# Performance work log

Hardware: AMD Instinct MI355X
Metric: run time of the kernel (lower is better)

## Reference

```python
import jax, jax.numpy as jnp
import numpy as np

V, OOV, E, HE, HD, B, S, T = 50000, 100, 128, 256, 256, 32, 256, 16
NEG = -1e20


def lstm(x, W, U, b, h0, c0):
    # x: [B, L, F]; standard (Keras-style i,f,g,o) LSTM via scan over time
    def step(carry, xt):
        h, c = carry
        z = xt @ W + h @ U + b
        i, f, g, o = jnp.split(z, 4, axis=-1)
        c = jax.nn.sigmoid(f) * c + jax.nn.sigmoid(i) * jnp.tanh(g)
        h = jax.nn.sigmoid(o) * jnp.tanh(c)
        return (h, c), h
    (h, c), hs = jax.lax.scan(step, (h0, c0), jnp.swapaxes(x, 0, 1))
    return jnp.swapaxes(hs, 0, 1), h, c


def setup_inputs() -> dict:
    key = jax.random.key(0)
    ks = jax.random.split(key, 16)
    g = lambda i, shape: jax.random.normal(ks[i], shape, dtype=jnp.float32) * 0.05
    return {
        'x': jax.random.randint(ks[0], (B, S), 0, V),
        'x_with_oov': jax.random.randint(ks[1], (B, S), 0, V + OOV),
        'x_len': jax.random.randint(ks[2], (B,), 1, S + 1),
        'dec_x': jax.random.randint(ks[3], (B, T), 0, V),
        'embedding': g(4, (V, E)),
        'Wenc': g(5, (E, 4 * HE)), 'Uenc': g(6, (HE, 4 * HE)), 'benc': jnp.zeros(4 * HE, jnp.float32),
        'We2d': g(7, (HE, HD)), 'be2d': jnp.zeros(HD, jnp.float32),
        'Wdec': g(8, (E, 4 * HD)), 'Udec': g(9, (HD, 4 * HD)), 'bdec': jnp.zeros(4 * HD, jnp.float32),
        'Wattn': g(10, (HD, HE)),
        'Wout': g(11, (HE + HD, HD)), 'bout': jnp.zeros(HD, jnp.float32),
        'Wgen': g(12, (HD, V)),
        'Wcopy': g(13, (HE, HD)), 'bcopy': jnp.zeros(HD, jnp.float32),
    }


def reference(x, x_with_oov, x_len, dec_x, embedding, Wenc, Uenc, benc,
              We2d, be2d, Wdec, Udec, bdec, Wattn, Wout, bout, Wgen, Wcopy, bcopy):
    # Encoder (unidirectional; Keras encoder ignores mask in this branch)
    enc_out, eh, ec = lstm(embedding[x], Wenc, Uenc, benc,
                           jnp.zeros((B, HE), embedding.dtype), jnp.zeros((B, HE), embedding.dtype))
    # NOTE: source applies encoder2decoder_state to BOTH h and c (faithful)
    h0 = eh @ We2d + be2d
    c0 = ec @ We2d + be2d
    # Decoder LSTM
    dec_out, sh, sc = lstm(embedding[dec_x], Wdec, Udec, bdec, h0, c0)  # [B,T,HD]
    mask = jnp.arange(S)[None, :] < x_len[:, None]                      # [B,S]
    # Attention (score_mode='general')
    scores = jnp.einsum('bth,he,bse->bts', dec_out, Wattn, enc_out)     # [B,T,S]
    scores = jnp.where(mask[:, None, :], scores, NEG)
    aw = jax.nn.softmax(scores, axis=2)
    ctx = jnp.einsum('bts,bse->bte', aw, enc_out)                       # [B,T,HE]
    attn_out = jnp.tanh(jnp.concatenate([ctx, dec_out], axis=-1) @ Wout + bout)  # [B,T,HD]
    # Generation scores, padded with tiny constant over OOV slots
    gen = jnp.exp(attn_out @ Wgen)                                      # [B,T,V]
    gen = jnp.pad(gen, ((0, 0), (0, 0), (0, OOV)), constant_values=1e-10)
    # Copy scores over source positions, scattered into extended vocab
    copy_seq = jnp.einsum('bsh,bth->bts', jnp.tanh(enc_out @ Wcopy + bcopy), attn_out)
    copy_seq = jnp.exp(jnp.where(mask[:, None, :], copy_seq, NEG))      # [B,T,S]
    b_idx = jnp.arange(B)[:, None, None]
    t_idx = jnp.arange(T)[None, :, None]
    v_idx = x_with_oov[:, None, :]                                      # broadcast to [B,T,S]
    copy_vocab = jnp.zeros((B, T, V + OOV), gen.dtype).at[b_idx, t_idx, v_idx].add(copy_seq)
    total = gen + copy_vocab
    log_prob = jnp.log(total / jnp.sum(total, axis=2, keepdims=True))
    return log_prob, sh, sc
```

## Files before the change

kernel.cpp:

```cpp
#include <hip/hip_runtime.h>

#define V_   50000
#define OOV_ 100
#define VO_  50100
#define E_   128
#define HE_  256
#define HD_  256
#define B_   32
#define S_   256
#define T_   16

typedef _Float16 h2_t __attribute__((ext_vector_type(2)));
typedef __attribute__((ext_vector_type(8))) short bfrag_t;
typedef __attribute__((ext_vector_type(4))) float f32x4;
typedef unsigned short ushort_t;

union U32H2 { unsigned u; h2_t h; };
union FRAG  { uint4 u; bfrag_t s; };

static __device__ __forceinline__ float bf2f(unsigned short b) {
  return __uint_as_float(((unsigned)b) << 16);
}
static __device__ __forceinline__ unsigned short f2bf(float f) {
  unsigned u = __float_as_uint(f);
  unsigned r = (u + 0x7fffu + ((u >> 16) & 1u)) >> 16;
  return (unsigned short)r;
}
static __device__ __forceinline__ float sigm(float x) { return 1.f / (1.f + expf(-x)); }

static __device__ __forceinline__ float dot2u(unsigned upair, unsigned hpairv, float acc) {
  U32H2 a; a.u = upair;
  U32H2 b; b.u = hpairv;
#if __has_builtin(__builtin_amdgcn_fdot2)
  return __builtin_amdgcn_fdot2(a.h, b.h, acc, false);
#else
  acc = fmaf((float)a.h.x, (float)b.h.x, acc);
  return fmaf((float)a.h.y, (float)b.h.y, acc);
#endif
}

__global__ __launch_bounds__(256) void mfma_gemm(
    const ushort_t* __restrict__ A, const ushort_t* __restrict__ Bt,
    const float* __restrict__ bias, float* __restrict__ C, ushort_t* __restrict__ Cbf,
    float* __restrict__ rsum, int M, int N, int K, int ldC, int act)
{
  const int w = threadIdx.x >> 6, lane = threadIdx.x & 63;
  const int m0 = blockIdx.y * 64 + w * 16;
  const int n0 = blockIdx.x * 64;
  const int l16 = lane & 15, lq = lane >> 4;
  f32x4 acc[4] = {f32x4{0,0,0,0}, f32x4{0,0,0,0}, f32x4{0,0,0,0}, f32x4{0,0,0,0}};
  for (int k0 = 0; k0 < K; k0 += 32) {
    FRAG a;
    a.u = *(const uint4*)(A + (size_t)(m0 + l16) * K + k0 + lq * 8);
#pragma unroll
    for (int ns = 0; ns < 4; ns++) {
      int n = n0 + ns * 16 + l16;
      int nc = n < N ? n : N - 1;
      FRAG bf;
      bf.u = *(const uint4*)(Bt + (size_t)nc * K + k0 + lq * 8);
      acc[ns] = __builtin_amdgcn_mfma_f32_16x16x32_bf16(a.s, bf.s, acc[ns], 0, 0, 0);
    }
  }
  float bv[4];
#pragma unroll
  for (int ns = 0; ns < 4; ns++) {
    int col = n0 + ns * 16 + l16;
    bv[ns] = (bias && col < N) ? bias[col] : 0.f;
  }
#pragma unroll
  for (int r = 0; r < 4; r++) {
    int row = m0 + lq * 4 + r;
    float part = 0.f;
#pragma unroll
    for (int ns = 0; ns < 4; ns++) {
      int col = n0 + ns * 16 + l16;
      if (col < N) {
        float v = acc[ns][r] + bv[ns];
        if (act == 1) v = tanhf(v);
        else if (act == 2) v = expf(v);
        if (Cbf) Cbf[(size_t)row * ldC + col] = f2bf(v);
        else     C[(size_t)row * ldC + col] = v;
        part += v;
      }
    }
    if (rsum) {
      part += __shfl_xor(part, 1);
      part += __shfl_xor(part, 2);
      part += __shfl_xor(part, 4);
      part += __shfl_xor(part, 8);
      if (l16 == 0) atomicAdd(&rsum[row], part);
    }
  }
}

static __device__ __forceinline__ void tconv_tile(
    const float* __restrict__ W, ushort_t* __restrict__ Wt, int K, int N,
    int kb, int nb, int tid, ushort_t (*tile)[33])
{
  const int tx = tid & 31, ty = tid >> 5;
#pragma unroll
  for (int p = 0; p < 4; p++) {
    int k = kb + ty + p * 8, n = nb + tx;
    if (k < K && n < N) tile[ty + p * 8][tx] = f2bf(W[(size_t)k * N + n]);
  }
  __syncthreads();
#pragma unroll
  for (int p = 0; p < 4; p++) {
    int n = nb + ty + p * 8, k = kb + tx;
    if (k < K && n < N) Wt[(size_t)n * K + k] = tile[tx][ty + p * 8];
  }
}
static __device__ __forceinline__ void packU2_one(
    const float* __restrict__ U, unsigned* __restrict__ out, int i)
{
  int p = i >> 10, col = i & 1023;
  U32H2 cv; cv.h = h2_t{(_Float16)U[(size_t)(2 * p) * 1024 + col],
                        (_Float16)U[(size_t)(2 * p + 1) * 1024 + col]};
  out[i] = cv.u;
}

__global__ __launch_bounds__(256) void prep_kernel(
    const float* __restrict__ Wenc, const float* __restrict__ Wdec,
    const float* __restrict__ We2d, const float* __restrict__ Wattn,
    const float* __restrict__ Wout, const float* __restrict__ Wcopy,
    const float* __restrict__ Uenc, const float* __restrict__ Udec,
    const int* __restrict__ x, const int* __restrict__ decx, const float* __restrict__ emb,
    ushort_t* WencT, ushort_t* WdecT, ushort_t* We2dT, ushort_t* WattnT,
    ushort_t* WoutT, ushort_t* WcopyT, unsigned* Upk2E, unsigned* Upk2D,
    ushort_t* xembbf, ushort_t* dembbf)
{
  __shared__ ushort_t tile[32][33];
  int blk = blockIdx.x;
  const int tid = threadIdx.x;
  if (blk < 128) { tconv_tile(Wenc, WencT, 128, 1024, (blk >> 5) * 32, (blk & 31) * 32, tid, tile); return; }
  blk -= 128;
  if (blk < 128) { tconv_tile(Wdec, WdecT, 128, 1024, (blk >> 5) * 32, (blk & 31) * 32, tid, tile); return; }
  blk -= 128;
  if (blk < 64)  { tconv_tile(We2d, We2dT, 256, 256, (blk >> 3) * 32, (blk & 7) * 32, tid, tile); return; }
  blk -= 64;
  if (blk < 64)  { tconv_tile(Wattn, WattnT, 256, 256, (blk >> 3) * 32, (blk & 7) * 32, tid, tile); return; }
  blk -= 64;
  if (blk < 128) { tconv_tile(Wout, WoutT, 512, 256, (blk >> 3) * 32, (blk & 7) * 32, tid, tile); return; }
  blk -= 128;
  if (blk < 64)  { tconv_tile(Wcopy, WcopyT, 256, 256, (blk >> 3) * 32, (blk & 7) * 32, tid, tile); return; }
  blk -= 64;
  if (blk < 512) { packU2_one(Uenc, Upk2E, blk * 256 + tid); return; }
  blk -= 512;
  if (blk < 512) { packU2_one(Udec, Upk2D, blk * 256 + tid); return; }
  blk -= 512;
  if (blk < 4096) {
    int i = blk * 256 + tid, r = i >> 7;
    xembbf[i] = f2bf(emb[(size_t)x[r] * E_ + (i & 127)]);
    return;
  }
  blk -= 4096;
  {
    int i = blk * 256 + tid, r = i >> 7;
    dembbf[i] = f2bf(emb[(size_t)decx[r] * E_ + (i & 127)]);
  }
}

#define DOT8(u0, u1, hpi)                \
  acc[0] = dot2u(u0.x, hpi, acc[0]);     \
  acc[1] = dot2u(u0.y, hpi, acc[1]);     \
  acc[2] = dot2u(u0.z, hpi, acc[2]);     \
  acc[3] = dot2u(u0.w, hpi, acc[3]);     \
  acc[4] = dot2u(u1.x, hpi, acc[4]);     \
  acc[5] = dot2u(u1.y, hpi, acc[5]);     \
  acc[6] = dot2u(u1.z, hpi, acc[6]);     \
  acc[7] = dot2u(u1.w, hpi, acc[7]);

__global__ __launch_bounds__(1024, 4) void lstm8(
    const float* __restrict__ Xpre, const unsigned* __restrict__ Upk2,
    const float* __restrict__ h0, const float* __restrict__ c0,
    ushort_t* __restrict__ outH, float* __restrict__ hN, float* __restrict__ cN,
    int steps, const float* __restrict__ Wg, ushort_t* __restrict__ WgT)
{
  __shared__ unsigned ldsU[8 * 4116];
  __shared__ float    zpart[4 * 1028];
  __shared__ float    actbuf[1024];
  __shared__ unsigned hpair[8 * 20];
  const int tid = threadIdx.x;

  if (blockIdx.x >= 32) {
    ushort_t* tile = (ushort_t*)ldsU;
    int tb = blockIdx.x - 32;
    int kb = (tb & 3) * 64, nb = (tb >> 2) * 64;
#pragma unroll
    for (int p = 0; p < 4; p++) {
      int i = p * 1024 + tid, k = i >> 6, n = i & 63;
      if (nb + n < V_) tile[k * 65 + n] = f2bf(Wg[(size_t)(kb + k) * V_ + nb + n]);
    }
    __syncthreads();
#pragma unroll
    for (int p = 0; p < 4; p++) {
      int i = p * 1024 + tid, n = i >> 6, k = i & 63;
      if (nb + n < V_) WgT[(size_t)(nb + n) * 256 + kb + k] = tile[k * 65 + n];
    }
    return;
  }

  const int b = blockIdx.x;
  const int jg = tid >> 3, kq = tid & 7;

  uint4 Ur[24];
  const unsigned* ubase = Upk2 + jg * 8;
#pragma unroll
  for (int i = 0; i < 12; i++) {
    int p = kq * 16 + i;
    Ur[2 * i]     = *(const uint4*)(ubase + p * 1024);
    Ur[2 * i + 1] = *(const uint4*)(ubase + p * 1024 + 4);
  }
#pragma unroll
  for (int i = 0; i < 4; i++) {
    int p = kq * 16 + 12 + i;
    uint4 q0 = *(const uint4*)(ubase + p * 1024);
    uint4 q1 = *(const uint4*)(ubase + p * 1024 + 4);
    *(uint4*)&ldsU[kq * 4116 + i * 1028 + jg * 8]     = q0;
    *(uint4*)&ldsU[kq * 4116 + i * 1028 + jg * 8 + 4] = q1;
  }
  float c = 0.f, hcur = 0.f;
  if (tid < 256) {
    c    = c0 ? c0[b * 256 + tid] : 0.f;
    hcur = h0 ? h0[b * 256 + tid] : 0.f;
  }
  if (tid < 128) {
    float a  = h0 ? h0[b * 256 + 2 * tid] : 0.f;
    float b2 = h0 ? h0[b * 256 + 2 * tid + 1] : 0.f;
    U32H2 cv; cv.h = h2_t{(_Float16)a, (_Float16)b2};
    hpair[(tid >> 4) * 20 + (tid & 15)] = cv.u;
  }
  __syncthreads();

  const float* xp = Xpre + (size_t)b * steps * 1024;
  const unsigned* myld = &ldsU[kq * 4116 + jg * 8];

  float xv = xp[tid];
  for (int t = 0; t < steps; t++) {
    float xvn = xp[(size_t)((t + 1 < steps) ? t + 1 : t) * 1024 + tid];
    float acc[8] = {0.f, 0.f, 0.f, 0.f, 0.f, 0.f, 0.f, 0.f};
    {
      uint4 hA = *(const uint4*)&hpair[kq * 20];
      DOT8(Ur[0], Ur[1], hA.x)  DOT8(Ur[2], Ur[3], hA.y)
      DOT8(Ur[4], Ur[5], hA.z)  DOT8(Ur[6], Ur[7], hA.w)
    }
    {
      uint4 hB = *(const uint4*)&hpair[kq * 20 + 4];
      DOT8(Ur[8], Ur[9], hB.x)   DOT8(Ur[10], Ur[11], hB.y)
      DOT8(Ur[12], Ur[13], hB.z) DOT8(Ur[14], Ur[15], hB.w)
    }
    {
      uint4 hC = *(const uint4*)&hpair[kq * 20 + 8];
      DOT8(Ur[16], Ur[17], hC.x) DOT8(Ur[18], Ur[19], hC.y)
      DOT8(Ur[20], Ur[21], hC.z) DOT8(Ur[22], Ur[23], hC.w)
    }
    {
      uint4 hD = *(const uint4*)&hpair[kq * 20 + 12];
      unsigned hh[4] = {hD.x, hD.y, hD.z, hD.w};
#pragma unroll
      for (int r = 0; r < 4; r++) {
        uint4 u0 = *(const uint4*)(myld + r * 1028);
        uint4 u1 = *(const uint4*)(myld + r * 1028 + 4);
        unsigned hpi = hh[r];
        DOT8(u0, u1, hpi)
      }
    }
#pragma unroll
    for (int g = 0; g < 8; g++) acc[g] += __shfl_xor(acc[g], 1);
    if ((kq & 1) == 0) {
      int r = kq >> 1;
      *(float4*)&zpart[r * 1028 + jg * 8]     = make_float4(acc[0], acc[1], acc[2], acc[3]);
      *(float4*)&zpart[r * 1028 + jg * 8 + 4] = make_float4(acc[4], acc[5], acc[6], acc[7]);
    }
    __syncthreads();
    float z = xv + zpart[tid] + zpart[1028 + tid] + zpart[2 * 1028 + tid] + zpart[3 * 1028 + tid];
    float av;
    if (tid >= 512 && tid < 768) {
      float e = __builtin_amdgcn_exp2f(-2.885390082f * z);
      av = 2.f * __builtin_amdgcn_rcpf(1.f + e) - 1.f;
    } else {
      float e = __builtin_amdgcn_exp2f(-1.442695041f * z);
      av = __builtin_amdgcn_rcpf(1.f + e);
    }
    actbuf[tid] = av;
    __syncthreads();
    if (tid < 256) {
      float ai = actbuf[tid], af = actbuf[tid + 256];
      float gg = actbuf[tid + 512], ao = actbuf[tid + 768];
      c = fmaf(af, c, ai * gg);
      float e2 = __builtin_amdgcn_exp2f(-2.885390082f * c);
      float th = 2.f * __builtin_amdgcn_rcpf(1.f + e2) - 1.f;
      hcur = ao * th;
      outH[((size_t)b * steps + t) * 256 + tid] = f2bf(hcur);
      float hnx = __shfl_down(hcur, 1);
      if ((tid & 1) == 0) {
        U32H2 cv; cv.h = h2_t{(_Float16)hcur, (_Float16)hnx};
        int P = tid >> 1;
        hpair[(P >> 4) * 20 + (P & 15)] = cv.u;
      }
    }
    xv = xvn;
    __syncthreads();
  }
  if (tid < 256) {
    hN[b * 256 + tid] = hcur;
    cN[b * 256 + tid] = c;
  }
}

__global__ __launch_bounds__(256) void attn_kernel(
    const float* __restrict__ dq, const ushort_t* __restrict__ enc,
    const int* __restrict__ x_len, float* __restrict__ ctx)
{
  __shared__ float q[256];
  __shared__ float eb[32][256];
  __shared__ float sc[256];
  __shared__ float red[8];
  const int bt = blockIdx.x, tid = threadIdx.x;
  const int b = bt >> 4;
  q[tid] = dq[(size_t)bt * 256 + tid];
  const int len = x_len[b];
  const unsigned* encu = (const unsigned*)(enc + (size_t)b * S_ * 256);
  __syncthreads();
  const int s_loc = tid >> 3, hb = (tid & 7) * 32;
  for (int cch = 0; cch < 8; cch++) {
#pragma unroll
    for (int qv = 0; qv < 16; qv++) {
      int idx = qv * 256 + tid;
      unsigned u = encu[cch * 4096 + idx];
      int row = idx >> 7, cp2 = (idx & 127) * 2;
      eb[row][cp2]     = bf2f((unsigned short)(u & 0xffffu));
      eb[row][cp2 + 1] = bf2f((unsigned short)(u >> 16));
    }
    __syncthreads();
    float p = 0.f;
#pragma unroll
    for (int h = 0; h < 32; h++) p = fmaf(q[hb + h], eb[s_loc][hb + h], p);
    p += __shfl_down(p, 4, 8);
    p += __shfl_down(p, 2, 8);
    p += __shfl_down(p, 1, 8);
    if ((tid & 7) == 0) sc[cch * 32 + s_loc] = p;
    __syncthreads();
  }
  float my = (tid < len) ? sc[tid] : -1e30f;
  float m = my;
#pragma unroll
  for (int o = 32; o >= 1; o >>= 1) m = fmaxf(m, __shfl_xor(m, o));
  if ((tid & 63) == 0) red[tid >> 6] = m;
  __syncthreads();
  float bm = fmaxf(fmaxf(red[0], red[1]), fmaxf(red[2], red[3]));
  float e = expf(my - bm);
  float s = e;
#pragma unroll
  for (int o = 32; o >= 1; o >>= 1) s += __shfl_xor(s, o);
  if ((tid & 63) == 0) red[4 + (tid >> 6)] = s;
  __syncthreads();
  float tot = red[4] + red[5] + red[6] + red[7];
  sc[tid] = e / tot;
  __syncthreads();
  const ushort_t* encb = enc + (size_t)b * S_ * 256;
  float acc = 0.f;
  for (int s2 = 0; s2 < 256; s2++) acc = fmaf(sc[s2], bf2f(encb[(size_t)s2 * 256 + tid]), acc);
  ctx[(size_t)bt * 256 + tid] = acc;
}

__global__ __launch_bounds__(256) void copyseq_kernel(
    const float* __restrict__ at, const ushort_t* __restrict__ cp,
    const int* __restrict__ x_len, float* __restrict__ cseq)
{
  __shared__ float q[256];
  __shared__ float eb[32][256];
  __shared__ float sc[256];
  const int bt = blockIdx.x, tid = threadIdx.x;
  const int b = bt >> 4;
  q[tid] = at[(size_t)bt * 256 + tid];
  const int len = x_len[b];
  const unsigned* cpu_ = (const unsigned*)(cp + (size_t)b * S_ * 256);
  __syncthreads();
  const int s_loc = tid >> 3, hb = (tid & 7) * 32;
  for (int cch = 0; cch < 8; cch++) {
#pragma unroll
    for (int qv = 0; qv < 16; qv++) {
      int idx = qv * 256 + tid;
      unsigned u = cpu_[cch * 4096 + idx];
      int row = idx >> 7, cp2 = (idx & 127) * 2;
      eb[row][cp2]     = bf2f((unsigned short)(u & 0xffffu));
      eb[row][cp2 + 1] = bf2f((unsigned short)(u >> 16));
    }
    __syncthreads();
    float p = 0.f;
#pragma unroll
    for (int h = 0; h < 32; h++) p = fmaf(q[hb + h], eb[s_loc][hb + h], p);
    p += __shfl_down(p, 4, 8);
    p += __shfl_down(p, 2, 8);
    p += __shfl_down(p, 1, 8);
    if ((tid & 7) == 0) sc[cch * 32 + s_loc] = p;
    __syncthreads();
  }
  cseq[(size_t)bt * 256 + tid] = (tid < len) ? expf(sc[tid]) : 0.f;
}

__global__ void f2bf_kernel(const float* __restrict__ in, ushort_t* __restrict__ out, int n) {
  int i = blockIdx.x * 256 + threadIdx.x;
  if (i < n) out[i] = f2bf(in[i]);
}
__global__ void concat_bf(const float* __restrict__ ctx, const ushort_t* __restrict__ dec,
                          ushort_t* __restrict__ cat) {
  int i = blockIdx.x * 256 + threadIdx.x;
  int r = i >> 9, j = i & 511;
  cat[i] = (j < 256) ? f2bf(ctx[r * 256 + j]) : dec[r * 256 + (j - 256)];
}
__global__ void pad_kernel(float* __restrict__ out) {
  int i = blockIdx.x * 256 + threadIdx.x;
  if (i < B_ * T_ * OOV_) {
    int bt = i / OOV_, j = i - bt * OOV_;
    out[(size_t)bt * VO_ + V_ + j] = 1e-10f;
  }
}
__global__ __launch_bounds__(256) void scatter_kernel(
    const float* __restrict__ cseq, const int* __restrict__ xoov,
    float* __restrict__ out, float* __restrict__ rsum)
{
  __shared__ float red[4];
  const int bt = blockIdx.x, tid = threadIdx.x, b = bt >> 4;
  float v = cseq[(size_t)bt * 256 + tid];
  if (v != 0.f) atomicAdd(&out[(size_t)bt * VO_ + xoov[b * S_ + tid]], v);
  float s = v;
#pragma unroll
  for (int o = 32; o >= 1; o >>= 1) s += __shfl_xor(s, o);
  if ((tid & 63) == 0) red[tid >> 6] = s;
  __syncthreads();
  if (tid == 0) atomicAdd(&rsum[bt], red[0] + red[1] + red[2] + red[3]);
}
__global__ void rowlog_kernel(const float* __restrict__ rsum, float* __restrict__ rowlog) {
  int i = blockIdx.x * 256 + threadIdx.x;
  if (i < B_ * T_) rowlog[i] = logf(rsum[i] + 1e-8f);
}
__global__ void finalize_kernel(float* __restrict__ out, const float* __restrict__ rowlog) {
  size_t i = (size_t)blockIdx.x * 256 + threadIdx.x;
  if (i < (size_t)B_ * T_ * VO_) {
    int bt = (int)(i / VO_);
    out[i] = logf(out[i]) - rowlog[bt];
  }
}

extern "C" void kernel_launch(void* const* d_in, const int* in_sizes, int n_in,
                              void* d_out, int out_size, void* d_ws, size_t ws_size,
                              hipStream_t stream) {
  const int*   x     = (const int*)d_in[0];
  const int*   xoov  = (const int*)d_in[1];
  const int*   xlen  = (const int*)d_in[2];
  const int*   decx  = (const int*)d_in[3];
  const float* emb   = (const float*)d_in[4];
  const float* Wenc  = (const float*)d_in[5];
  const float* Uenc  = (const float*)d_in[6];
  const float* benc  = (const float*)d_in[7];
  const float* We2d  = (const float*)d_in[8];
  const float* be2d  = (const float*)d_in[9];
  const float* Wdec  = (const float*)d_in[10];
  const float* Udec  = (const float*)d_in[11];
  const float* bdec  = (const float*)d_in[12];
  const float* Wattn = (const float*)d_in[13];
  const float* Wout  = (const float*)d_in[14];
  const float* bout  = (const float*)d_in[15];
  const float* Wgen  = (const float*)d_in[16];
  const float* Wcopy = (const float*)d_in[17];
  const float* bcopy = (const float*)d_in[18];
  float* out = (float*)d_out;
  float* ws  = (float*)d_ws;

  float*    Xenc   = ws + 0;
  ushort_t* WgenT  = (ushort_t*)(ws + 0);
  ushort_t* cp_bf  = (ushort_t*)(ws + 6400000);
  float*    dqb    = ws + 8388608;
  float*    ctxb   = ws + 8519680;
  float*    attno  = ws + 8650752;
  float*    cseq   = ws + 8781824;
  float*    rsum   = ws + 8912896;
  float*    rowlog = ws + 8913408;
  ushort_t* Abf    = (ushort_t*)(ws + 8913920);
  ushort_t* catb   = (ushort_t*)(ws + 8979456);
  ushort_t* decObf = (ushort_t*)(ws + 9110528);
  ushort_t* xembbf = (ushort_t*)(ws + 9176064);
  ushort_t* dembbf = (ushort_t*)(ws + 9700352);
  float*    Xdec   = ws + 9733120;
  ushort_t* WencT  = (ushort_t*)(ws + 10257408);
  ushort_t* WdecT  = (ushort_t*)(ws + 10322944);
  ushort_t* We2dT  = (ushort_t*)(ws + 10388480);
  ushort_t* WattnT = (ushort_t*)(ws + 10421248);
  ushort_t* WoutT  = (ushort_t*)(ws + 10454016);
  ushort_t* WcopyT = (ushort_t*)(ws + 10519552);
  unsigned* Upk2E  = (unsigned*)(ws + 10552320);
  unsigned* Upk2D  = (unsigned*)(ws + 10683392);
  ushort_t* encObf = (ushort_t*)(ws + 10814464);
  float*    ehc    = ws + 11863040;
  ushort_t* ehcbf  = (ushort_t*)(ws + 11879424);
  float*    h0c0   = ws + 11887616;

  float* sh  = out + (size_t)B_ * T_ * VO_;
  float* scf = sh + B_ * HD_;

  hipMemsetAsync(rsum, 0, 512 * sizeof(float), stream);

  hipLaunchKernelGGL(prep_kernel, dim3(5952), dim3(256), 0, stream,
                     Wenc, Wdec, We2d, Wattn, Wout, Wcopy, Uenc, Udec, x, decx, emb,
                     WencT, WdecT, We2dT, WattnT, WoutT, WcopyT, Upk2E, Upk2D,
                     xembbf, dembbf);

  hipLaunchKernelGGL(mfma_gemm, dim3(16, 128), dim3(256), 0, stream,
                     xembbf, WencT, benc, Xenc, (ushort_t*)nullptr, (float*)nullptr,
                     B_ * S_, 1024, 128, 1024, 0);
  hipLaunchKernelGGL(mfma_gemm, dim3(16, 8), dim3(256), 0, stream,
                     dembbf, WdecT, bdec, Xdec, (ushort_t*)nullptr, (float*)nullptr,
                     B_ * T_, 1024, 128, 1024, 0);

  hipLaunchKernelGGL(lstm8, dim3(32), dim3(1024), 0, stream,
                     Xenc, Upk2E, (const float*)nullptr, (const float*)nullptr,
                     encObf, ehc, ehc + 32 * 256, S_,
                     (const float*)nullptr, (ushort_t*)nullptr);

  hipLaunchKernelGGL(f2bf_kernel, dim3(64), dim3(256), 0, stream, ehc, ehcbf, 64 * 256);
  hipLaunchKernelGGL(mfma_gemm, dim3(4, 1), dim3(256), 0, stream,
                     ehcbf, We2dT, be2d, h0c0, (ushort_t*)nullptr, (float*)nullptr,
                     64, 256, 256, 256, 0);

  hipLaunchKernelGGL(lstm8, dim3(32 + 3128), dim3(1024), 0, stream,
                     Xdec, Upk2D, h0c0, h0c0 + 32 * 256, decObf, sh, scf, T_,
                     Wgen, WgenT);

  hipLaunchKernelGGL(mfma_gemm, dim3(4, 8), dim3(256), 0, stream,
                     decObf, WattnT, (const float*)nullptr, dqb, (ushort_t*)nullptr,
                     (float*)nullptr, B_ * T_, 256, 256, 256, 0);
  hipLaunchKernelGGL(attn_kernel, dim3(B_ * T_), dim3(256), 0, stream, dqb, encObf, xlen, ctxb);
  hipLaunchKernelGGL(concat_bf, dim3(1024), dim3(256), 0, stream, ctxb, decObf, catb);
  hipLaunchKernelGGL(mfma_gemm, dim3(4, 8), dim3(256), 0, stream,
                     catb, WoutT, bout, attno, (ushort_t*)nullptr, (float*)nullptr,
                     B_ * T_, 256, 512, 256, 1);
  hipLaunchKernelGGL(f2bf_kernel, dim3(512), dim3(256), 0, stream, attno, Abf, B_ * T_ * 256);
  hipLaunchKernelGGL(mfma_gemm, dim3(4, 128), dim3(256), 0, stream,
                     encObf, WcopyT, bcopy, (float*)nullptr, cp_bf, (float*)nullptr,
                     B_ * S_, 256, 256, 256, 1);
  hipLaunchKernelGGL(mfma_gemm, dim3(782, 8), dim3(256), 0, stream,
                     Abf, WgenT, (const float*)nullptr, out, (ushort_t*)nullptr, rsum,
                     B_ * T_, V_, 256, VO_, 2);
  hipLaunchKernelGGL(pad_kernel, dim3(200), dim3(256), 0, stream, out);
  hipLaunchKernelGGL(copyseq_kernel, dim3(B_ * T_), dim3(256), 0, stream, attno, cp_bf, xlen, cseq);
  hipLaunchKernelGGL(scatter_kernel, dim3(512), dim3(256), 0, stream, cseq, xoov, out, rsum);
  hipLaunchKernelGGL(rowlog_kernel, dim3(2), dim3(256), 0, stream, rsum, rowlog);
  hipLaunchKernelGGL(finalize_kernel, dim3((B_ * T_ * VO_ + 255) / 256), dim3(256), 0, stream,
                     out, rowlog);
}
```

Before: 1.193 ms.

## Fuse LSTM gate activations into one phase and fold small conversion kernels

The LSTM step now has 256 threads each compute all four gate sums and activations directly from the partial sums. This drops the activation buffer and one barrier per timestep on the serial critical path. The f2bf, concat and pad kernels are folded into the LSTM epilogue, the attention kernel, the GEMM's bf16 output and the scatter kernel, which removes several launches. In exchange, gate activation work is serialized onto a quarter of the threads, and copyseq now reads a bf16 attention output instead of fp32.

```diff
diff --git a/kernel.cpp b/kernel.cpp
--- a/kernel.cpp
+++ b/kernel.cpp
@@ -27,6 +27,14 @@
   return (unsigned short)r;
 }
 static __device__ __forceinline__ float sigm(float x) { return 1.f / (1.f + expf(-x)); }
+static __device__ __forceinline__ float fast_sigm(float z) {
+  float e = __builtin_amdgcn_exp2f(-1.442695041f * z);
+  return __builtin_amdgcn_rcpf(1.f + e);
+}
+static __device__ __forceinline__ float fast_tanh(float z) {
+  float e = __builtin_amdgcn_exp2f(-2.885390082f * z);
+  return 2.f * __builtin_amdgcn_rcpf(1.f + e) - 1.f;
+}
 
 static __device__ __forceinline__ float dot2u(unsigned upair, unsigned hpairv, float acc) {
   U32H2 a; a.u = upair;
@@ -170,15 +178,15 @@
   acc[6] = dot2u(u1.z, hpi, acc[6]);     \
   acc[7] = dot2u(u1.w, hpi, acc[7]);
 
-__global__ __launch_bounds__(1024, 4) void lstm8(
+__global__ __launch_bounds__(1024, 4) void lstm9(
     const float* __restrict__ Xpre, const unsigned* __restrict__ Upk2,
     const float* __restrict__ h0, const float* __restrict__ c0,
     ushort_t* __restrict__ outH, float* __restrict__ hN, float* __restrict__ cN,
+    ushort_t* __restrict__ hNbf, ushort_t* __restrict__ cNbf,
     int steps, const float* __restrict__ Wg, ushort_t* __restrict__ WgT)
 {
   __shared__ unsigned ldsU[8 * 4116];
   __shared__ float    zpart[4 * 1028];
-  __shared__ float    actbuf[1024];
   __shared__ unsigned hpair[8 * 20];
   const int tid = threadIdx.x;
 
@@ -235,9 +243,12 @@
   const float* xp = Xpre + (size_t)b * steps * 1024;
   const unsigned* myld = &ldsU[kq * 4116 + jg * 8];
 
-  float xv = xp[tid];
   for (int t = 0; t < steps; t++) {
-    float xvn = xp[(size_t)((t + 1 < steps) ? t + 1 : t) * 1024 + tid];
+    float xq0 = 0.f, xq1 = 0.f, xq2 = 0.f, xq3 = 0.f;
+    if (tid < 256) {
+      const float* xr = xp + (size_t)t * 1024 + tid;
+      xq0 = xr[0]; xq1 = xr[256]; xq2 = xr[512]; xq3 = xr[768];
+    }
     float acc[8] = {0.f, 0.f, 0.f, 0.f, 0.f, 0.f, 0.f, 0.f};
     {
       uint4 hA = *(const uint4*)&hpair[kq * 20];
@@ -273,24 +284,17 @@
       *(float4*)&zpart[r * 1028 + jg * 8 + 4] = make_float4(acc[4], acc[5], acc[6], acc[7]);
     }
     __syncthreads();
-    float z = xv + zpart[tid] + zpart[1028 + tid] + zpart[2 * 1028 + tid] + zpart[3 * 1028 + tid];
-    float av;
-    if (tid >= 512 && tid < 768) {
-      float e = __builtin_amdgcn_exp2f(-2.885390082f * z);
-      av = 2.f * __builtin_amdgcn_rcpf(1.f + e) - 1.f;
-    } else {
-      float e = __builtin_amdgcn_exp2f(-1.442695041f * z);
-      av = __builtin_amdgcn_rcpf(1.f + e);
-    }
-    actbuf[tid] = av;
-    __syncthreads();
     if (tid < 256) {
-      float ai = actbuf[tid], af = actbuf[tid + 256];
-      float gg = actbuf[tid + 512], ao = actbuf[tid + 768];
-      c = fmaf(af, c, ai * gg);
-      float e2 = __builtin_amdgcn_exp2f(-2.885390082f * c);
-      float th = 2.f * __builtin_amdgcn_rcpf(1.f + e2) - 1.f;
-      hcur = ao * th;
+      float zi = xq0, zf = xq1, zg = xq2, zo = xq3;
+#pragma unroll
+      for (int r = 0; r < 4; r++) {
+        const float* zr = &zpart[r * 1028 + tid];
+        zi += zr[0]; zf += zr[256]; zg += zr[512]; zo += zr[768];
+      }
+      float ai = fast_sigm(zi), af = fast_sigm(zf);
+      float ag = fast_tanh(zg), ao = fast_sigm(zo);
+      c = fmaf(af, c, ai * ag);
+      hcur = ao * fast_tanh(c);
       outH[((size_t)b * steps + t) * 256 + tid] = f2bf(hcur);
       float hnx = __shfl_down(hcur, 1);
       if ((tid & 1) == 0) {
@@ -299,18 +303,20 @@
         hpair[(P >> 4) * 20 + (P & 15)] = cv.u;
       }
     }
-    xv = xvn;
     __syncthreads();
   }
   if (tid < 256) {
-    hN[b * 256 + tid] = hcur;
-    cN[b * 256 + tid] = c;
+    if (hN)   hN[b * 256 + tid] = hcur;
+    if (cN)   cN[b * 256 + tid] = c;
+    if (hNbf) hNbf[b * 256 + tid] = f2bf(hcur);
+    if (cNbf) cNbf[b * 256 + tid] = f2bf(c);
   }
 }
 
 __global__ __launch_bounds__(256) void attn_kernel(
     const float* __restrict__ dq, const ushort_t* __restrict__ enc,
-    const int* __restrict__ x_len, float* __restrict__ ctx)
+    const int* __restrict__ x_len, const ushort_t* __restrict__ dec,
+    ushort_t* __restrict__ catb)
 {
   __shared__ float q[256];
   __shared__ float eb[32][256];
@@ -361,11 +367,12 @@
   const ushort_t* encb = enc + (size_t)b * S_ * 256;
   float acc = 0.f;
   for (int s2 = 0; s2 < 256; s2++) acc = fmaf(sc[s2], bf2f(encb[(size_t)s2 * 256 + tid]), acc);
-  ctx[(size_t)bt * 256 + tid] = acc;
+  catb[(size_t)bt * 512 + tid]       = f2bf(acc);
+  catb[(size_t)bt * 512 + 256 + tid] = dec[(size_t)bt * 256 + tid];
 }
 
 __global__ __launch_bounds__(256) void copyseq_kernel(
-    const float* __restrict__ at, const ushort_t* __restrict__ cp,
+    const ushort_t* __restrict__ at, const ushort_t* __restrict__ cp,
     const int* __restrict__ x_len, float* __restrict__ cseq)
 {
   __shared__ float q[256];
@@ -373,7 +380,7 @@
   __shared__ float sc[256];
   const int bt = blockIdx.x, tid = threadIdx.x;
   const int b = bt >> 4;
-  q[tid] = at[(size_t)bt * 256 + tid];
+  q[tid] = bf2f(at[(size_t)bt * 256 + tid]);
   const int len = x_len[b];
   const unsigned* cpu_ = (const unsigned*)(cp + (size_t)b * S_ * 256);
   __syncthreads();
@@ -400,29 +407,14 @@
   cseq[(size_t)bt * 256 + tid] = (tid < len) ? expf(sc[tid]) : 0.f;
 }
 
-__global__ void f2bf_kernel(const float* __restrict__ in, ushort_t* __restrict__ out, int n) {
-  int i = blockIdx.x * 256 + threadIdx.x;
-  if (i < n) out[i] = f2bf(in[i]);
-}
-__global__ void concat_bf(const float* __restrict__ ctx, const ushort_t* __restrict__ dec,
-                          ushort_t* __restrict__ cat) {
-  int i = blockIdx.x * 256 + threadIdx.x;
-  int r = i >> 9, j = i & 511;
-  cat[i] = (j < 256) ? f2bf(ctx[r * 256 + j]) : dec[r * 256 + (j - 256)];
-}
-__global__ void pad_kernel(float* __restrict__ out) {
-  int i = blockIdx.x * 256 + threadIdx.x;
-  if (i < B_ * T_ * OOV_) {
-    int bt = i / OOV_, j = i - bt * OOV_;
-    out[(size_t)bt * VO_ + V_ + j] = 1e-10f;
-  }
-}
 __global__ __launch_bounds__(256) void scatter_kernel(
     const float* __restrict__ cseq, const int* __restrict__ xoov,
     float* __restrict__ out, float* __restrict__ rsum)
 {
   __shared__ float red[4];
   const int bt = blockIdx.x, tid = threadIdx.x, b = bt >> 4;
+  if (tid < OOV_) out[(size_t)bt * VO_ + V_ + tid] = 1e-10f;
+  __syncthreads();
   float v = cseq[(size_t)bt * 256 + tid];
   if (v != 0.f) atomicAdd(&out[(size_t)bt * VO_ + xoov[b * S_ + tid]], v);
   float s = v;
@@ -473,8 +465,6 @@
   ushort_t* WgenT  = (ushort_t*)(ws + 0);
   ushort_t* cp_bf  = (ushort_t*)(ws + 6400000);
   float*    dqb    = ws + 8388608;
-  float*    ctxb   = ws + 8519680;
-  float*    attno  = ws + 8650752;
   float*    cseq   = ws + 8781824;
   float*    rsum   = ws + 8912896;
   float*    rowlog = ws + 8913408;
@@ -514,37 +504,36 @@
                      dembbf, WdecT, bdec, Xdec, (ushort_t*)nullptr, (float*)nullptr,
                      B_ * T_, 1024, 128, 1024, 0);
 
-  hipLaunchKernelGGL(lstm8, dim3(32), dim3(1024), 0, stream,
+  hipLaunchKernelGGL(lstm9, dim3(32), dim3(1024), 0, stream,
                      Xenc, Upk2E, (const float*)nullptr, (const float*)nullptr,
-                     encObf, ehc, ehc + 32 * 256, S_,
+                     encObf, (float*)nullptr, (float*)nullptr,
+                     ehcbf, ehcbf + 32 * 256, S_,
                      (const float*)nullptr, (ushort_t*)nullptr);
 
-  hipLaunchKernelGGL(f2bf_kernel, dim3(64), dim3(256), 0, stream, ehc, ehcbf, 64 * 256);
   hipLaunchKernelGGL(mfma_gemm, dim3(4, 1), dim3(256), 0, stream,
                      ehcbf, We2dT, be2d, h0c0, (ushort_t*)nullptr, (float*)nullptr,
                      64, 256, 256, 256, 0);
 
-  hipLaunchKernelGGL(lstm8, dim3(32 + 3128), dim3(1024), 0, stream,
-                     Xdec, Upk2D, h0c0, h0c0 + 32 * 256, decObf, sh, scf, T_,
+  hipLaunchKernelGGL(lstm9, dim3(32 + 3128), dim3(1024), 0, stream,
+                     Xdec, Upk2D, h0c0, h0c0 + 32 * 256, decObf, sh, scf,
+                     (ushort_t*)nullptr, (ushort_t*)nullptr, T_,
                      Wgen, WgenT);
 
   hipLaunchKernelGGL(mfma_gemm, dim3(4, 8), dim3(256), 0, stream,
                      decObf, WattnT, (const float*)nullptr, dqb, (ushort_t*)nullptr,
                      (float*)nullptr, B_ * T_, 256, 256, 256, 0);
-  hipLaunchKernelGGL(attn_kernel, dim3(B_ * T_), dim3(256), 0, stream, dqb, encObf, xlen, ctxb);
-  hipLaunchKernelGGL(concat_bf, dim3(1024), dim3(256), 0, stream, ctxb, decObf, catb);
+  hipLaunchKernelGGL(attn_kernel, dim3(B_ * T_), dim3(256), 0, stream,
+                     dqb, encObf, xlen, decObf, catb);
   hipLaunchKernelGGL(mfma_gemm, dim3(4, 8), dim3(256), 0, stream,
-                     catb, WoutT, bout, attno, (ushort_t*)nullptr, (float*)nullptr,
+                     catb, WoutT, bout, (float*)nullptr, Abf, (float*)nullptr,
                      B_ * T_, 256, 512, 256, 1);
-  hipLaunchKernelGGL(f2bf_kernel, dim3(512), dim3(256), 0, stream, attno, Abf, B_ * T_ * 256);
   hipLaunchKernelGGL(mfma_gemm, dim3(4, 128), dim3(256), 0, stream,
                      encObf, WcopyT, bcopy, (float*)nullptr, cp_bf, (float*)nullptr,
                      B_ * S_, 256, 256, 256, 1);
   hipLaunchKernelGGL(mfma_gemm, dim3(782, 8), dim3(256), 0, stream,
                      Abf, WgenT, (const float*)nullptr, out, (ushort_t*)nullptr, rsum,
                      B_ * T_, V_, 256, VO_, 2);
-  hipLaunchKernelGGL(pad_kernel, dim3(200), dim3(256), 0, stream, out);
-  hipLaunchKernelGGL(copyseq_kernel, dim3(B_ * T_), dim3(256), 0, stream, attno, cp_bf, xlen, cseq);
+  hipLaunchKernelGGL(copyseq_kernel, dim3(B_ * T_), dim3(256), 0, stream, Abf, cp_bf, xlen, cseq);
   hipLaunchKernelGGL(scatter_kernel, dim3(512), dim3(256), 0, stream, cseq, xoov, out, rsum);
   hipLaunchKernelGGL(rowlog_kernel, dim3(2), dim3(256), 0, stream, rsum, rowlog);
   hipLaunchKernelGGL(finalize_kernel, dim3((B_ * T_ * VO_ + 255) / 256), dim3(256), 0, stream,
```

New measurement: 1.203 ms. No clear change (+0.8%).
